# Optimization experiments

Hardware: AMD Instinct MI355X
Metric: run time of the kernel (lower is better)

Reference implementation:

```python
import jax, jax.numpy as jnp
import numpy as np

B, M, L, HID, H, LAYERS = 16, 128, 512, 256, 4, 2
DH = HID // H  # 64 = head dim, also kernel_param dim


def _ln(x, g, b, eps=1e-5):
    mu = jnp.mean(x, axis=-1, keepdims=True)
    var = jnp.mean((x - mu) ** 2, axis=-1, keepdims=True)
    return (x - mu) / jnp.sqrt(var + eps) * g + b


def setup_inputs() -> dict:
    key = jax.random.key(0)
    ks = jax.random.split(key, 24)
    s = 0.05
    return {
        "ct_t": jax.random.uniform(ks[0], (B, M), jnp.float32),
        "ts_t": jax.random.uniform(ks[1], (B, L), jnp.float32),
        "ct_emb": jax.random.normal(ks[2], (B, M, HID), jnp.float32),
        "ts_emb": jax.random.normal(ks[3], (B, L, HID), jnp.float32),
        "kernel_param": jax.random.normal(ks[4], (DH,), jnp.float32),
        "ct_W": jax.random.normal(ks[5], (HID, HID), jnp.float32) * s,
        "ct_b": jnp.zeros((HID,), jnp.float32),
        "fW0": jax.random.normal(ks[6], (HID, HID), jnp.float32) * s,
        "fb0": jnp.zeros((HID,), jnp.float32),
        "fW1": jax.random.normal(ks[7], (HID, HID), jnp.float32) * s,
        "fb1": jnp.zeros((HID,), jnp.float32),
        "fW2": jax.random.normal(ks[8], (HID, HID), jnp.float32) * s,
        "fb2": jnp.zeros((HID,), jnp.float32),
        "f_ln_g": jnp.ones((HID,), jnp.float32),
        "f_ln_b": jnp.zeros((HID,), jnp.float32),
        "Wqkv": jax.random.normal(ks[9], (LAYERS, 3 * HID, HID), jnp.float32) * s,
        "bqkv": jnp.zeros((LAYERS, 3 * HID), jnp.float32),
        "Wo": jax.random.normal(ks[10], (LAYERS, HID, HID), jnp.float32) * s,
        "bo": jnp.zeros((LAYERS, HID), jnp.float32),
        "W1": jax.random.normal(ks[11], (LAYERS, 2 * HID, HID), jnp.float32) * s,
        "b1": jnp.zeros((LAYERS, 2 * HID), jnp.float32),
        "W2": jax.random.normal(ks[12], (LAYERS, HID, 2 * HID), jnp.float32) * s,
        "b2": jnp.zeros((LAYERS, HID), jnp.float32),
        "ln1_g": jnp.ones((LAYERS, HID), jnp.float32),
        "ln1_b": jnp.zeros((LAYERS, HID), jnp.float32),
        "ln2_g": jnp.ones((LAYERS, HID), jnp.float32),
        "ln2_b": jnp.zeros((LAYERS, HID), jnp.float32),
        "pred_W": jax.random.normal(ks[13], (1, HID), jnp.float32) * s,
        "pred_b": jnp.zeros((1,), jnp.float32),
    }


def reference(ct_t, ts_t, ct_emb, ts_emb, kernel_param, ct_W, ct_b,
              fW0, fb0, fW1, fb1, fW2, fb2, f_ln_g, f_ln_b,
              Wqkv, bqkv, Wo, bo, W1, b1, W2, b2,
              ln1_g, ln1_b, ln2_g, ln2_b, pred_W, pred_b):
    # --- TN tokenizer: multi-scale RBF kernel temporal fusion ---
    alpha = jax.nn.softplus(kernel_param)                       # [DH]  log(1+exp(p))
    ct_e = (jnp.einsum('bmd,ed->bme', ct_emb, ct_W) + ct_b)     # [B,M,HID]
    ct_e = ct_e.reshape(B, M, H, DH)
    diff = ct_t[:, :, None] - ts_t[:, None, :]                  # [B,M,L]
    norm = (diff * diff)[..., None]                             # [B,M,L,1]
    outs = []
    for s in range(H):                                          # fixed small loop over scales
        z = (-float(s)) * alpha * norm                          # [B,M,L,DH]
        w = jax.nn.logsumexp(z, axis=3, keepdims=True)          # [B,M,L,1]
        sim = jnp.exp(z - w)                                    # normalized kernel sims
        outs.append(jnp.einsum('bmnd,bmd->bnd', sim, ct_e[:, :, s, :]))  # scatter over ts events
    temp = jnp.concatenate(outs, axis=-1)                       # [B,L,HID]
    # --- Fusion module ---
    aux = jax.nn.elu(temp @ fW0.T + fb0 + ts_emb @ fW1.T + fb1)
    x = _ln(aux @ fW2.T + fb2 + ts_emb, f_ln_g, f_ln_b)         # [B,L,HID]
    # --- Transformer encoder (post-LN, gelu, no dropout at eval) ---
    inv_sqrt = 1.0 / np.sqrt(DH).astype(np.float32)
    for l in range(LAYERS):
        qkv = x @ Wqkv[l].T + bqkv[l]                           # [B,L,3*HID]
        q, k, v = jnp.split(qkv, 3, axis=-1)
        def heads(t):
            return t.reshape(B, L, H, DH).transpose(0, 2, 1, 3)
        q, k, v = heads(q), heads(k), heads(v)
        att = jax.nn.softmax(jnp.einsum('bhqd,bhkd->bhqk', q, k) * inv_sqrt, axis=-1)
        o = jnp.einsum('bhqk,bhkd->bhqd', att, v).transpose(0, 2, 1, 3).reshape(B, L, HID)
        x = _ln(x + o @ Wo[l].T + bo[l], ln1_g[l], ln1_b[l])
        ff = jax.nn.gelu(x @ W1[l].T + b1[l], approximate=False) @ W2[l].T + b2[l]
        x = _ln(x + ff, ln2_g[l], ln2_b[l])
    return x @ pred_W.T + pred_b                                # [B,L,1]
```

## Files before the change

### kernel.cpp

```cpp
#include <hip/hip_runtime.h>
#include <hip/hip_bf16.h>
#include <cstddef>

#define Bsz 16
#define Msz 128
#define Lsz 512
#define HIDs 256

typedef __attribute__((ext_vector_type(4))) float f32x4;
typedef __attribute__((ext_vector_type(8))) __bf16 bf16x8;
typedef __attribute__((ext_vector_type(8))) unsigned short ushort8;

#define CHEB_K 12
#define PI_F 3.14159265358979323846f

static __device__ inline unsigned short f2bf(float f) {
    __hip_bfloat16 h = __float2bfloat16(f);
    return *(unsigned short*)&h;
}
static __device__ inline float bf2f(unsigned short u) {
    return __builtin_bit_cast(float, (unsigned)u << 16);
}
static __device__ inline void gload16(const ushort* g, ushort* l) {
    __builtin_amdgcn_global_load_lds(
        (const __attribute__((address_space(1))) void*)g,
        (__attribute__((address_space(3))) void*)l, 16, 0, 0);
}

__global__ __launch_bounds__(256) void cheb_kernel(
    const float* __restrict__ kp, float* __restrict__ clut, float* __restrict__ cD)
{
    __shared__ float costab[CHEB_K][32];
    __shared__ float xq[32];
    __shared__ float alph[64];
    const int t = threadIdx.x;
    if (t < 64) {
        float p = kp[t];
        alph[t] = fmaxf(p, 0.f) + log1pf(__expf(-fabsf(p)));
    }
    #pragma unroll
    for (int i = 0; i < 2; i++) {
        int idx = i * 256 + t;
        if (idx < CHEB_K * 32) {
            int k = idx >> 5, q = idx & 31;
            float th = (q + 0.5f) * (PI_F / 32.f);
            costab[k][q] = __cosf((float)k * th);
        }
    }
    if (t < 32) xq[t] = 0.5f * (1.f + __cosf((t + 0.5f) * (PI_F / 32.f)));
    __syncthreads();

    if (t >= 192) return;
    const int d = t & 63, s1 = t >> 6;
    const float u = (float)(s1 + 1) * alph[d];
    float f[32];
    #pragma unroll
    for (int q = 0; q < 32; q++) f[q] = __expf(-u * xq[q]);
    #pragma unroll
    for (int k = 0; k < CHEB_K; k++) {
        float sum = 0.f;
        #pragma unroll
        for (int q = 0; q < 32; q++) sum = fmaf(f[q], costab[k][q], sum);
        float c = sum * ((k == 0 ? 1.f : 2.f) / 32.f);
        clut[s1 * (CHEB_K * 64) + k * 64 + d] = c;
        float sr = c;
        #pragma unroll
        for (int o = 1; o <= 32; o <<= 1) sr += __shfl_xor(sr, o, 64);
        if (d == 0) cD[s1 * CHEB_K + k] = sr;
    }
}

__global__ __launch_bounds__(256) void prep_kernel(
    const float* __restrict__ ts_emb, const float* __restrict__ ct_emb,
    const float* __restrict__ ct_W, const float* __restrict__ fW0,
    const float* __restrict__ fW1, const float* __restrict__ fW2,
    const float* __restrict__ Wqkv, const float* __restrict__ Wo,
    const float* __restrict__ W1, const float* __restrict__ W2,
    ushort* __restrict__ Xcat, ushort* __restrict__ Wcat,
    ushort* __restrict__ cebin, ushort* __restrict__ wct,
    ushort* __restrict__ wf2, ushort* __restrict__ wqkv,
    ushort* __restrict__ wo, ushort* __restrict__ w1, ushort* __restrict__ w2,
    const float* __restrict__ ct_t, const float* __restrict__ ts_t,
    const float* __restrict__ cD, ushort* __restrict__ invW,
    const float* __restrict__ bqkv, float* __restrict__ bqs)
{
    const int bid = blockIdx.x;
    const int tid = threadIdx.x;

    if (bid < 1920) {
        const unsigned u = bid * 256u + tid;
        const float* src; ushort* dst; unsigned rel;
        float sc = 1.f;
        if (u < 262144u) {
            rel = u; src = ts_emb;
            dst = Xcat + ((size_t)(rel >> 5) * 512 + 256 + (rel & 31) * 8);
        } else if (u < 327680u) { rel = u - 262144u; src = ct_emb; dst = cebin + (size_t)rel * 8; }
        else if (u < 335872u) { rel = u - 327680u; src = ct_W; dst = wct + (size_t)rel * 8; }
        else if (u < 344064u) { rel = u - 335872u; src = fW0;
            dst = Wcat + ((size_t)(rel >> 5) * 512 + (rel & 31) * 8); }
        else if (u < 352256u) { rel = u - 344064u; src = fW1;
            dst = Wcat + ((size_t)(rel >> 5) * 512 + 256 + (rel & 31) * 8); }
        else if (u < 360448u) { rel = u - 352256u; src = fW2; dst = wf2 + (size_t)rel * 8; }
        else if (u < 409600u) { rel = u - 360448u; src = Wqkv; dst = wqkv + (size_t)rel * 8;
            if (((rel >> 5) % 768) < 256) sc = 0.125f; }
        else if (u < 425984u) { rel = u - 409600u; src = Wo;  dst = wo + (size_t)rel * 8; }
        else if (u < 458752u) { rel = u - 425984u; src = W1;  dst = w1 + (size_t)rel * 8; }
        else                  { rel = u - 458752u; src = W2;  dst = w2 + (size_t)rel * 8; }
        float4 a = ((const float4*)src)[(size_t)rel * 2];
        float4 b = ((const float4*)src)[(size_t)rel * 2 + 1];
        ushort8 o;
        o[0] = f2bf(a.x * sc); o[1] = f2bf(a.y * sc); o[2] = f2bf(a.z * sc); o[3] = f2bf(a.w * sc);
        o[4] = f2bf(b.x * sc); o[5] = f2bf(b.y * sc); o[6] = f2bf(b.z * sc); o[7] = f2bf(b.w * sc);
        *(ushort8*)dst = o;
    } else if (bid < 6016) {
        __shared__ float cd[3][CHEB_K];
        if (tid < 3 * CHEB_K) cd[tid / CHEB_K][tid % CHEB_K] = cD[tid];
        __syncthreads();

        const unsigned G = (bid - 1920) * 256u + tid;
        const int b = G >> 16;
        const int n = (G >> 7) & 511;
        const int m = G & 127;

        float x = ct_t[b * Msz + m] - ts_t[b * Lsz + n];
        x = x * x;
        const float xi = 2.f * x - 1.f;
        const float xi2 = 2.f * xi;

        float t0 = 1.f, t1 = xi;
        float a1 = cd[0][0] + cd[0][1] * xi;
        float a2 = cd[1][0] + cd[1][1] * xi;
        float a3 = cd[2][0] + cd[2][1] * xi;
        #pragma unroll
        for (int k = 2; k < CHEB_K; k++) {
            float tn = fmaf(xi2, t1, -t0);
            a1 = fmaf(cd[0][k], tn, a1);
            a2 = fmaf(cd[1][k], tn, a2);
            a3 = fmaf(cd[2][k], tn, a3);
            t0 = t1; t1 = tn;
        }
        const size_t base = ((size_t)b * 3 * Lsz + n) * Msz + m;
        invW[base]                         = f2bf(1.f / a1);
        invW[base + (size_t)Lsz * Msz]     = f2bf(1.f / a2);
        invW[base + (size_t)2 * Lsz * Msz] = f2bf(1.f / a3);
    } else {
        #pragma unroll
        for (int i = 0; i < 6; i++) {
            int idx = i * 256 + tid;
            int c = idx % 768;
            bqs[idx] = bqkv[idx] * ((c < 256) ? 0.125f : 1.f);
        }
    }
}

__global__ __launch_bounds__(256) void gemm_mfma_kernel(
    const ushort* __restrict__ X, const ushort* __restrict__ W,
    const float* __restrict__ bias, const float* __restrict__ bias2,
    ushort* __restrict__ Yb, int NR, int K, int OUT, int act)
{
    __shared__ ushort As[2][64 * 64];
    __shared__ ushort Bs[2][128 * 64];

    const int nbx = OUT >> 7;
    const int bx = blockIdx.x % nbx;
    const int by = blockIdx.x / nbx;
    const int r0 = by << 6, o0 = bx << 7;
    const int tid = threadIdx.x;
    const int w = tid >> 6;
    const int lane = tid & 63;
    const int wr = w >> 1, wc = w & 1;
    const int lr = lane & 15, lg = lane >> 4;

    const int grow = lane >> 3;
    const int gchunk = (lane & 7) ^ grow;

    unsigned aoff[2][2], boff[4][2];
    #pragma unroll
    for (int f = 0; f < 2; f++) {
        unsigned cc = (unsigned)((lg + 4 * f) ^ (lr & 7)) * 16u;
        #pragma unroll
        for (int m = 0; m < 2; m++)
            aoff[m][f] = (unsigned)(wr * 32 + m * 16 + lr) * 128u + cc;
        #pragma unroll
        for (int n = 0; n < 4; n++)
            boff[n][f] = (unsigned)(wc * 64 + n * 16 + lr) * 128u + cc;
    }

    f32x4 acc[2][4];
    #pragma unroll
    for (int m = 0; m < 2; m++)
        #pragma unroll
        for (int n = 0; n < 4; n++) acc[m][n] = (f32x4){0.f, 0.f, 0.f, 0.f};

    const int nk = K >> 6;

    auto stage = [&](int buf, int ks) {
        const int k0 = ks << 6;
        #pragma unroll
        for (int i = 0; i < 2; i++) {
            int row = w * 16 + i * 8 + grow;
            gload16(X + (size_t)(r0 + row) * K + k0 + gchunk * 8,
                    &As[buf][(w * 16 + i * 8) * 64]);
        }
        #pragma unroll
        for (int i = 0; i < 4; i++) {
            int row = w * 32 + i * 8 + grow;
            gload16(W + (size_t)(o0 + row) * K + k0 + gchunk * 8,
                    &Bs[buf][(w * 32 + i * 8) * 64]);
        }
    };

    stage(0, 0);
    __syncthreads();
    int cur = 0;
    for (int ks = 0; ks < nk; ks++) {
        if (ks + 1 < nk) stage(cur ^ 1, ks + 1);
        const char* Ab = (const char*)As[cur];
        const char* Bb = (const char*)Bs[cur];
        #pragma unroll
        for (int f = 0; f < 2; f++) {
            bf16x8 av[2], bv[4];
            #pragma unroll
            for (int m = 0; m < 2; m++)
                av[m] = *(const bf16x8*)(Ab + aoff[m][f]);
            #pragma unroll
            for (int n = 0; n < 4; n++)
                bv[n] = *(const bf16x8*)(Bb + boff[n][f]);
            #pragma unroll
            for (int m = 0; m < 2; m++)
                #pragma unroll
                for (int n = 0; n < 4; n++)
                    acc[m][n] = __builtin_amdgcn_mfma_f32_16x16x32_bf16(
                        av[m], bv[n], acc[m][n], 0, 0, 0);
        }
        __syncthreads();
        cur ^= 1;
    }

    const int ocol0 = o0 + wc * 64;
    float bn[4];
    #pragma unroll
    for (int n = 0; n < 4; n++) {
        int o = ocol0 + n * 16 + lr;
        bn[n] = bias[o] + (bias2 ? bias2[o] : 0.f);
    }

    #pragma unroll
    for (int m = 0; m < 2; m++) {
        #pragma unroll
        for (int p = 0; p < 4; p++) {
            int r = r0 + wr * 32 + m * 16 + 4 * lg + p;
            size_t rb = (size_t)r * OUT;
            #pragma unroll
            for (int n = 0; n < 4; n++) {
                int o = ocol0 + n * 16 + lr;
                float v = acc[m][n][p] + bn[n];
                if (act == 1)      v = (v > 0.f) ? v : (__expf(v) - 1.f);
                else if (act == 2) v = 0.5f * v * (1.f + erff(v * 0.70710678118654752f));
                Yb[rb + o] = f2bf(v);
            }
        }
    }
}

__global__ __launch_bounds__(256) void gemm_ln_kernel(
    const ushort* __restrict__ X, const ushort* __restrict__ W,
    const float* __restrict__ bias, const ushort* __restrict__ add,
    int addS, int addO,
    const float* __restrict__ lng, const float* __restrict__ lnb,
    ushort* __restrict__ Xb,
    const float* __restrict__ predW, const float* __restrict__ predb,
    float* __restrict__ pout, int K)
{
    __shared__ ushort As[2][16 * 64];
    __shared__ ushort Bs[2][256 * 64];
    __shared__ float redA[16][4];
    __shared__ float redB[16][4];

    const int r0 = blockIdx.x << 4;
    const int tid = threadIdx.x;
    const int w = tid >> 6;
    const int lane = tid & 63;
    const int lr = lane & 15, lg = lane >> 4;
    const int grow = lane >> 3;
    const int gchunk = (lane & 7) ^ grow;

    unsigned aoff[2], boff[4][2];
    #pragma unroll
    for (int f = 0; f < 2; f++) {
        unsigned cc = (unsigned)((lg + 4 * f) ^ (lr & 7)) * 16u;
        aoff[f] = (unsigned)lr * 128u + cc;
        #pragma unroll
        for (int n = 0; n < 4; n++)
            boff[n][f] = (unsigned)(w * 64 + n * 16 + lr) * 128u + cc;
    }

    f32x4 acc[4];
    #pragma unroll
    for (int n = 0; n < 4; n++) acc[n] = (f32x4){0.f, 0.f, 0.f, 0.f};

    const int nk = K >> 6;

    auto stage = [&](int buf, int ks) {
        const int k0 = ks << 6;
        if (w < 2)
            gload16(X + (size_t)(r0 + w * 8 + grow) * K + k0 + gchunk * 8,
                    &As[buf][(w * 8) * 64]);
        #pragma unroll
        for (int i = 0; i < 8; i++) {
            gload16(W + (size_t)(w * 64 + i * 8 + grow) * K + k0 + gchunk * 8,
                    &Bs[buf][(w * 64 + i * 8) * 64]);
        }
    };

    stage(0, 0);
    __syncthreads();
    int cur = 0;
    for (int ks = 0; ks < nk; ks++) {
        if (ks + 1 < nk) stage(cur ^ 1, ks + 1);
        const char* Ab = (const char*)As[cur];
        const char* Bb = (const char*)Bs[cur];
        #pragma unroll
        for (int f = 0; f < 2; f++) {
            bf16x8 av = *(const bf16x8*)(Ab + aoff[f]);
            #pragma unroll
            for (int n = 0; n < 4; n++) {
                bf16x8 bv = *(const bf16x8*)(Bb + boff[n][f]);
                acc[n] = __builtin_amdgcn_mfma_f32_16x16x32_bf16(
                    av, bv, acc[n], 0, 0, 0);
            }
        }
        __syncthreads();
        cur ^= 1;
    }

    const int col0 = w * 64;
    float bn[4], gv[4], bv2[4], pwv[4];
    #pragma unroll
    for (int n = 0; n < 4; n++) {
        int o = col0 + n * 16 + lr;
        bn[n] = bias[o];
        gv[n] = lng[o];
        bv2[n] = lnb[o];
        pwv[n] = predW ? predW[o] : 0.f;
    }
    #pragma unroll
    for (int p = 0; p < 4; p++) {
        size_t ra = (size_t)(r0 + 4 * lg + p) * addS + addO;
        #pragma unroll
        for (int n = 0; n < 4; n++)
            acc[n][p] += bn[n] + bf2f(add[ra + col0 + n * 16 + lr]);
    }

    #pragma unroll
    for (int p = 0; p < 4; p++) {
        float s = acc[0][p] + acc[1][p] + acc[2][p] + acc[3][p];
        #pragma unroll
        for (int o = 1; o <= 8; o <<= 1) s += __shfl_xor(s, o);
        if (lr == 0) redA[4 * lg + p][w] = s;
    }
    __syncthreads();
    float mu[4];
    #pragma unroll
    for (int p = 0; p < 4; p++) {
        int row = 4 * lg + p;
        mu[p] = (redA[row][0] + redA[row][1] + redA[row][2] + redA[row][3]) * (1.f / 256.f);
    }

    #pragma unroll
    for (int p = 0; p < 4; p++) {
        float q = 0.f;
        #pragma unroll
        for (int n = 0; n < 4; n++) {
            float dl = acc[n][p] - mu[p];
            q = fmaf(dl, dl, q);
        }
        #pragma unroll
        for (int o = 1; o <= 8; o <<= 1) q += __shfl_xor(q, o);
        if (lr == 0) redB[4 * lg + p][w] = q;
    }
    __syncthreads();

    #pragma unroll
    for (int p = 0; p < 4; p++) {
        int row = 4 * lg + p;
        float var = (redB[row][0] + redB[row][1] + redB[row][2] + redB[row][3]) * (1.f / 256.f);
        float rsig = rsqrtf(var + 1e-5f);
        size_t rb = (size_t)(r0 + row) * 256;
        float pd = 0.f;
        #pragma unroll
        for (int n = 0; n < 4; n++) {
            int o = col0 + n * 16 + lr;
            float xn = (acc[n][p] - mu[p]) * rsig * gv[n] + bv2[n];
            if (Xb) Xb[rb + o] = f2bf(xn);
            pd = fmaf(xn, pwv[n], pd);
        }
        if (predW) {
            #pragma unroll
            for (int o = 1; o <= 8; o <<= 1) pd += __shfl_xor(pd, o);
            if (lr == 0) redA[row][w] = pd;
        }
    }
    if (predW) {
        __syncthreads();
        if (tid < 16)
            pout[r0 + tid] = redA[tid][0] + redA[tid][1] + redA[tid][2]
                           + redA[tid][3] + predb[0];
    }
}

__global__ __launch_bounds__(256) void tokmix_kernel(
    const float* __restrict__ ct_t, const float* __restrict__ ts_t,
    const ushort* __restrict__ ceb, const ushort* __restrict__ invW,
    const float* __restrict__ clut, ushort* __restrict__ Xcat)
{
    const int bid = blockIdx.x;
    const int tid = threadIdx.x;

    if (bid < 384) {
        const int nt = bid & 7;
        const int s1 = (bid >> 3) % 3;
        const int b  = bid / 24;
        const int w = tid >> 6, lane = tid & 63, g = lane >> 4, r = lane & 15;

        __shared__ ushort ceT[64][136];
        __shared__ float  cl[CHEB_K][64];
        __shared__ float  cts[128];

        #pragma unroll
        for (int i = 0; i < 8; i++) {
            int idx = i * 256 + tid;
            int m = idx >> 4, d4 = (idx & 15) << 2;
            const ushort* gp = ceb + (((size_t)b * 128 + m) << 8) + (s1 + 1) * 64 + d4;
            ushort4 v = *(const ushort4*)gp;
            ceT[d4 + 0][m] = v.x; ceT[d4 + 1][m] = v.y;
            ceT[d4 + 2][m] = v.z; ceT[d4 + 3][m] = v.w;
        }
        #pragma unroll
        for (int i = 0; i < 3; i++) {
            int idx = i * 256 + tid;
            cl[idx >> 6][idx & 63] = clut[s1 * (CHEB_K * 64) + idx];
        }
        if (tid < 128) cts[tid] = ct_t[b * 128 + tid];
        __syncthreads();

        const int nrow = nt * 64 + w * 16 + r;
        const float tsn = ts_t[b * 512 + nrow];

        float xi2v[4][8], Ta[4][8], Tb[4][8];
        #pragma unroll
        for (int t4 = 0; t4 < 4; t4++) {
            int m0 = 8 * g + 32 * t4;
            ushort8 iv = *(const ushort8*)&invW[((((size_t)b * 3 + s1) * 512 + nrow) << 7) + m0];
            #pragma unroll
            for (int j = 0; j < 8; j++) {
                float dfx = cts[m0 + j] - tsn;
                float x = dfx * dfx;
                float xi = 2.f * x - 1.f;
                float w0 = bf2f(iv[j]);
                xi2v[t4][j] = 2.f * xi;
                Ta[t4][j] = w0;
                Tb[t4][j] = w0 * xi;
            }
        }

        bf16x8 cef[4][4];
        #pragma unroll
        for (int db = 0; db < 4; db++)
            #pragma unroll
            for (int t4 = 0; t4 < 4; t4++)
                cef[db][t4] = *(const bf16x8*)&ceT[db * 16 + r][8 * g + 32 * t4];

        f32x4 acc[4];
        #pragma unroll
        for (int db = 0; db < 4; db++) acc[db] = (f32x4){0.f, 0.f, 0.f, 0.f};

        #pragma unroll
        for (int k = 0; k < CHEB_K; k++) {
            if (k >= 2) {
                #pragma unroll
                for (int t4 = 0; t4 < 4; t4++)
                    #pragma unroll
                    for (int j = 0; j < 8; j++) {
                        if (k & 1) Tb[t4][j] = fmaf(xi2v[t4][j], Ta[t4][j], -Tb[t4][j]);
                        else       Ta[t4][j] = fmaf(xi2v[t4][j], Tb[t4][j], -Ta[t4][j]);
                    }
            }
            bf16x8 af[4];
            #pragma unroll
            for (int t4 = 0; t4 < 4; t4++) {
                ushort8 u;
                #pragma unroll
                for (int j = 0; j < 8; j++)
                    u[j] = f2bf((k & 1) ? Tb[t4][j] : Ta[t4][j]);
                af[t4] = __builtin_bit_cast(bf16x8, u);
            }
            #pragma unroll
            for (int db = 0; db < 4; db++) {
                f32x4 gk = (f32x4){0.f, 0.f, 0.f, 0.f};
                #pragma unroll
                for (int t4 = 0; t4 < 4; t4++)
                    gk = __builtin_amdgcn_mfma_f32_16x16x32_bf16(af[t4], cef[db][t4], gk, 0, 0, 0);
                float ck = cl[k][db * 16 + r];
                #pragma unroll
                for (int p = 0; p < 4; p++) acc[db][p] = fmaf(ck, gk[p], acc[db][p]);
            }
        }

        #pragma unroll
        for (int db = 0; db < 4; db++)
            #pragma unroll
            for (int p = 0; p < 4; p++) {
                int n_out = nt * 64 + w * 16 + 4 * g + p;
                Xcat[((size_t)b * 512 + n_out) * 512 + (s1 + 1) * 64 + db * 16 + r] =
                    f2bf(acc[db][p]);
            }
    } else {
        const int b = bid - 384;
        const int d = tid & 63, q = tid >> 6;
        float s = 0.f;
        #pragma unroll 8
        for (int i = 0; i < 32; i++) {
            int m = q * 32 + i;
            s += bf2f(ceb[(((size_t)b * 128 + m) << 8) + d]);
        }
        __shared__ float red0[4][64];
        __shared__ ushort row0[64];
        red0[q][d] = s;
        __syncthreads();
        if (tid < 64)
            row0[tid] = f2bf((red0[0][tid] + red0[1][tid] + red0[2][tid] + red0[3][tid])
                             * (1.f / 64.f));
        __syncthreads();
        #pragma unroll
        for (int i = 0; i < 16; i++) {
            int idx = i * 256 + tid;
            int n = idx >> 3, j = idx & 7;
            *(ushort8*)&Xcat[((size_t)b * 512 + n) * 512 + j * 8] =
                *(const ushort8*)&row0[j * 8];
        }
    }
}

__global__ __launch_bounds__(256) void attn_mfma_kernel(
    const ushort* __restrict__ qkv, ushort* __restrict__ Ob)
{
    const int bid = blockIdx.x;
    const int qt = bid & 7;
    const int h  = (bid >> 3) & 3;
    const int b  = bid >> 5;
    const int t  = threadIdx.x;
    const int w  = t >> 6;
    const int lane = t & 63;
    const int g = lane >> 4;
    const int r = lane & 15;

    __shared__ ushort Ks[64][72];
    __shared__ ushort Vt[64][72];
    __shared__ float  Ps[4][16][65];

    const ushort* base = qkv + (size_t)b * Lsz * 768;
    const int q0 = qt * 64 + w * 16;

    bf16x8 qf[2];
    {
        const ushort* qp = base + (size_t)(q0 + r) * 768 + h * 64 + 8 * g;
        qf[0] = __builtin_bit_cast(bf16x8, *(const ushort8*)qp);
        qf[1] = __builtin_bit_cast(bf16x8, *(const ushort8*)(qp + 32));
    }

    f32x4 Ofr[4];
    #pragma unroll
    for (int dblk = 0; dblk < 4; dblk++) Ofr[dblk] = (f32x4){0.f, 0.f, 0.f, 0.f};
    float m_run[4] = {-1e30f, -1e30f, -1e30f, -1e30f};
    float l_run[4] = {0.f, 0.f, 0.f, 0.f};

    const int srow = t >> 2;
    const int sseg = t & 3;

    ushort8 pk0, pk1, pv0, pv1;
    auto gload_chunk = [&](int c) {
        const ushort* kr = base + (size_t)(c * 64 + srow) * 768 + 256 + h * 64 + sseg * 16;
        pk0 = *(const ushort8*)kr;
        pk1 = *(const ushort8*)(kr + 8);
        pv0 = *(const ushort8*)(kr + 256);
        pv1 = *(const ushort8*)(kr + 264);
    };
    auto write_chunk = [&]() {
        *(ushort8*)&Ks[srow][sseg * 16]     = pk0;
        *(ushort8*)&Ks[srow][sseg * 16 + 8] = pk1;
        #pragma unroll
        for (int j = 0; j < 8; j++) {
            Vt[sseg * 16 + j][srow]     = pv0[j];
            Vt[sseg * 16 + 8 + j][srow] = pv1[j];
        }
    };

    gload_chunk(0);
    write_chunk();
    __syncthreads();

    for (int c = 0; c < 8; c++) {
        if (c < 7) gload_chunk(c + 1);

        f32x4 sfr[4];
        #pragma unroll
        for (int s = 0; s < 4; s++) {
            f32x4 a2 = (f32x4){0.f, 0.f, 0.f, 0.f};
            #pragma unroll
            for (int f = 0; f < 2; f++) {
                bf16x8 kf = *(const bf16x8*)&Ks[s * 16 + r][8 * g + 32 * f];
                a2 = __builtin_amdgcn_mfma_f32_16x16x32_bf16(qf[f], kf, a2, 0, 0, 0);
            }
            sfr[s] = a2;
        }

        #pragma unroll
        for (int p = 0; p < 4; p++) {
            float rm = fmaxf(fmaxf(sfr[0][p], sfr[1][p]), fmaxf(sfr[2][p], sfr[3][p]));
            #pragma unroll
            for (int o = 1; o <= 8; o <<= 1) rm = fmaxf(rm, __shfl_xor(rm, o));
            float mnew = fmaxf(m_run[p], rm);
            float sc = __expf(m_run[p] - mnew);
            m_run[p] = mnew;
            float rs = 0.f;
            #pragma unroll
            for (int s = 0; s < 4; s++) {
                float pv = __expf(sfr[s][p] - mnew);
                Ps[w][4 * g + p][s * 16 + r] = pv;
                rs += pv;
            }
            #pragma unroll
            for (int o = 1; o <= 8; o <<= 1) rs += __shfl_xor(rs, o);
            l_run[p] = l_run[p] * sc + rs;
            #pragma unroll
            for (int dblk = 0; dblk < 4; dblk++) Ofr[dblk][p] *= sc;
        }

        __asm__ volatile("s_waitcnt lgkmcnt(0)" ::: "memory");

        #pragma unroll
        for (int f = 0; f < 2; f++) {
            const float* pp = &Ps[w][r][8 * g + 32 * f];
            ushort8 ua;
            #pragma unroll
            for (int j = 0; j < 8; j++) ua[j] = f2bf(pp[j]);
            bf16x8 pa = __builtin_bit_cast(bf16x8, ua);
            #pragma unroll
            for (int dblk = 0; dblk < 4; dblk++) {
                bf16x8 vb = *(const bf16x8*)&Vt[dblk * 16 + r][32 * f + 8 * g];
                Ofr[dblk] = __builtin_amdgcn_mfma_f32_16x16x32_bf16(
                    pa, vb, Ofr[dblk], 0, 0, 0);
            }
        }

        __syncthreads();
        if (c < 7) {
            write_chunk();
            __syncthreads();
        }
    }

    #pragma unroll
    for (int dblk = 0; dblk < 4; dblk++) {
        #pragma unroll
        for (int p = 0; p < 4; p++) {
            int row = q0 + 4 * g + p;
            Ob[(size_t)(b * Lsz + row) * HIDs + h * 64 + dblk * 16 + r] =
                f2bf(Ofr[dblk][p] / l_run[p]);
        }
    }
}

extern "C" void kernel_launch(void* const* d_in, const int* in_sizes, int n_in,
                              void* d_out, int out_size, void* d_ws, size_t ws_size,
                              hipStream_t stream)
{
    (void)in_sizes; (void)n_in; (void)out_size; (void)ws_size;

    const float* ct_t   = (const float*)d_in[0];
    const float* ts_t   = (const float*)d_in[1];
    const float* ct_emb = (const float*)d_in[2];
    const float* ts_emb = (const float*)d_in[3];
    const float* kp     = (const float*)d_in[4];
    const float* ct_W   = (const float*)d_in[5];
    const float* ct_b   = (const float*)d_in[6];
    const float* fW0    = (const float*)d_in[7];
    const float* fb0    = (const float*)d_in[8];
    const float* fW1    = (const float*)d_in[9];
    const float* fb1    = (const float*)d_in[10];
    const float* fW2    = (const float*)d_in[11];
    const float* fb2    = (const float*)d_in[12];
    const float* f_ln_g = (const float*)d_in[13];
    const float* f_ln_b = (const float*)d_in[14];
    const float* Wqkv   = (const float*)d_in[15];
    const float* bqkv   = (const float*)d_in[16];
    const float* Wo     = (const float*)d_in[17];
    const float* bo     = (const float*)d_in[18];
    const float* W1     = (const float*)d_in[19];
    const float* b1     = (const float*)d_in[20];
    const float* W2     = (const float*)d_in[21];
    const float* b2     = (const float*)d_in[22];
    const float* ln1_g  = (const float*)d_in[23];
    const float* ln1_b  = (const float*)d_in[24];
    const float* ln2_g  = (const float*)d_in[25];
    const float* ln2_b  = (const float*)d_in[26];
    const float* pred_W = (const float*)d_in[27];
    const float* pred_b = (const float*)d_in[28];

    ushort* wsb = (ushort*)d_ws;
    ushort* invW  = wsb;
    ushort* auxbf = wsb;
    ushort* qkvbf = wsb;
    ushort* ff1bf = wsb;
    ushort* Xcat  = wsb + 12582912;
    ushort* Wcat  = wsb + 16777216;
    ushort* cebin = wsb + 16908288;
    ushort* cebout= wsb + 17432576;
    ushort* wct   = wsb + 17956864;
    ushort* wf2   = wsb + 18022400;
    ushort* wqkv  = wsb + 18087936;
    ushort* wo    = wsb + 18481152;
    ushort* w1    = wsb + 18612224;
    ushort* w2    = wsb + 18874368;
    ushort* xbf   = wsb + 19136512;
    ushort* obf   = wsb + 21233664;
    float*  wsf   = (float*)d_ws;
    float*  clut  = wsf + 11665408;
    float*  cDp   = wsf + 11667712;
    float*  bqs   = wsf + 11667776;

    const int NRts = Bsz * Lsz;
    const int NRct = Bsz * Msz;
    auto grid = [](int nr, int out) { return dim3((unsigned)((nr >> 6) * (out >> 7))); };

    cheb_kernel<<<dim3(1), 256, 0, stream>>>(kp, clut, cDp);
    prep_kernel<<<dim3(1920 + 4096 + 1), 256, 0, stream>>>(
        ts_emb, ct_emb, ct_W, fW0, fW1, fW2, Wqkv, Wo, W1, W2,
        Xcat, Wcat, cebin, wct, wf2, wqkv, wo, w1, w2,
        ct_t, ts_t, cDp, invW, bqkv, bqs);

    gemm_mfma_kernel<<<grid(NRct, 256), 256, 0, stream>>>(
        cebin, wct, ct_b, nullptr, cebout, NRct, 256, 256, 0);
    tokmix_kernel<<<dim3(400), 256, 0, stream>>>(ct_t, ts_t, cebout, invW, clut, Xcat);

    gemm_mfma_kernel<<<grid(NRts, 256), 256, 0, stream>>>(
        Xcat, Wcat, fb0, fb1, auxbf, NRts, 512, 256, 1);
    gemm_ln_kernel<<<dim3(NRts / 16), 256, 0, stream>>>(
        auxbf, wf2, fb2, Xcat, 512, 256, f_ln_g, f_ln_b, xbf,
        nullptr, nullptr, nullptr, 256);

    for (int l = 0; l < 2; l++) {
        gemm_mfma_kernel<<<grid(NRts, 768), 256, 0, stream>>>(
            xbf, wqkv + (size_t)l * 196608, bqs + l * 768, nullptr,
            qkvbf, NRts, 256, 768, 0);
        attn_mfma_kernel<<<dim3(512), 256, 0, stream>>>(qkvbf, obf);
        gemm_ln_kernel<<<dim3(NRts / 16), 256, 0, stream>>>(
            obf, wo + (size_t)l * 65536, bo + l * 256, xbf, 256, 0,
            ln1_g + l * 256, ln1_b + l * 256, xbf,
            nullptr, nullptr, nullptr, 256);
        gemm_mfma_kernel<<<grid(NRts, 512), 256, 0, stream>>>(
            xbf, w1 + (size_t)l * 131072, b1 + l * 512, nullptr,
            ff1bf, NRts, 256, 512, 2);
        if (l == 0) {
            gemm_ln_kernel<<<dim3(NRts / 16), 256, 0, stream>>>(
                ff1bf, w2 + (size_t)l * 131072, b2 + l * 256, xbf, 256, 0,
                ln2_g + l * 256, ln2_b + l * 256, xbf,
                nullptr, nullptr, nullptr, 512);
        } else {
            gemm_ln_kernel<<<dim3(NRts / 16), 256, 0, stream>>>(
                ff1bf, w2 + (size_t)l * 131072, b2 + l * 256, xbf, 256, 0,
                ln2_g + l * 256, ln2_b + l * 256, nullptr,
                pred_W, pred_b, (float*)d_out, 512);
        }
    }
}
```

Measured before the change: 197.5 us.

## Enlarge gemm_ln row tile to 32 and attention key chunks to 128

The fused GEMM+LayerNorm kernel now handles 32 rows per block with 512 threads. Two groups of four waves share each staged weight tile, which halves the redundant weight loads per row. The attention kernel now processes 128-key chunks in 4 iterations instead of 64-key chunks in 8, cutting loop and barrier overhead. It also raises wave priority around the MFMA sections. In exchange, LDS use grows in both kernels, which may lower occupancy, and the gemm_ln grid has half as many blocks.

```diff
diff --git a/kernel.cpp b/kernel.cpp
--- a/kernel.cpp
+++ b/kernel.cpp
@@ -263,7 +263,7 @@
     }
 }
 
-__global__ __launch_bounds__(256) void gemm_ln_kernel(
+__global__ __launch_bounds__(512) void gemm_ln_kernel(
     const ushort* __restrict__ X, const ushort* __restrict__ W,
     const float* __restrict__ bias, const ushort* __restrict__ add,
     int addS, int addO,
@@ -272,16 +272,18 @@
     const float* __restrict__ predW, const float* __restrict__ predb,
     float* __restrict__ pout, int K)
 {
-    __shared__ ushort As[2][16 * 64];
+    __shared__ ushort As[2][32 * 64];
     __shared__ ushort Bs[2][256 * 64];
-    __shared__ float redA[16][4];
-    __shared__ float redB[16][4];
-
-    const int r0 = blockIdx.x << 4;
+    __shared__ float redA[32][4];
+    __shared__ float redB[32][4];
+
+    const int r0 = blockIdx.x << 5;
     const int tid = threadIdx.x;
     const int w = tid >> 6;
     const int lane = tid & 63;
     const int lr = lane & 15, lg = lane >> 4;
+    const int wg = w >> 2;
+    const int ws = w & 3;
     const int grow = lane >> 3;
     const int gchunk = (lane & 7) ^ grow;
 
@@ -289,10 +291,10 @@
     #pragma unroll
     for (int f = 0; f < 2; f++) {
         unsigned cc = (unsigned)((lg + 4 * f) ^ (lr & 7)) * 16u;
-        aoff[f] = (unsigned)lr * 128u + cc;
+        aoff[f] = (unsigned)(wg * 16 + lr) * 128u + cc;
         #pragma unroll
         for (int n = 0; n < 4; n++)
-            boff[n][f] = (unsigned)(w * 64 + n * 16 + lr) * 128u + cc;
+            boff[n][f] = (unsigned)(ws * 64 + n * 16 + lr) * 128u + cc;
     }
 
     f32x4 acc[4];
@@ -303,13 +305,13 @@
 
     auto stage = [&](int buf, int ks) {
         const int k0 = ks << 6;
-        if (w < 2)
+        if (w < 4)
             gload16(X + (size_t)(r0 + w * 8 + grow) * K + k0 + gchunk * 8,
                     &As[buf][(w * 8) * 64]);
         #pragma unroll
-        for (int i = 0; i < 8; i++) {
-            gload16(W + (size_t)(w * 64 + i * 8 + grow) * K + k0 + gchunk * 8,
-                    &Bs[buf][(w * 64 + i * 8) * 64]);
+        for (int i = 0; i < 4; i++) {
+            gload16(W + (size_t)(w * 32 + i * 8 + grow) * K + k0 + gchunk * 8,
+                    &Bs[buf][(w * 32 + i * 8) * 64]);
         }
     };
 
@@ -334,7 +336,7 @@
         cur ^= 1;
     }
 
-    const int col0 = w * 64;
+    const int col0 = ws * 64;
     float bn[4], gv[4], bv2[4], pwv[4];
     #pragma unroll
     for (int n = 0; n < 4; n++) {
@@ -346,7 +348,7 @@
     }
     #pragma unroll
     for (int p = 0; p < 4; p++) {
-        size_t ra = (size_t)(r0 + 4 * lg + p) * addS + addO;
+        size_t ra = (size_t)(r0 + wg * 16 + 4 * lg + p) * addS + addO;
         #pragma unroll
         for (int n = 0; n < 4; n++)
             acc[n][p] += bn[n] + bf2f(add[ra + col0 + n * 16 + lr]);
@@ -357,13 +359,13 @@
         float s = acc[0][p] + acc[1][p] + acc[2][p] + acc[3][p];
         #pragma unroll
         for (int o = 1; o <= 8; o <<= 1) s += __shfl_xor(s, o);
-        if (lr == 0) redA[4 * lg + p][w] = s;
+        if (lr == 0) redA[wg * 16 + 4 * lg + p][ws] = s;
     }
     __syncthreads();
     float mu[4];
     #pragma unroll
     for (int p = 0; p < 4; p++) {
-        int row = 4 * lg + p;
+        int row = wg * 16 + 4 * lg + p;
         mu[p] = (redA[row][0] + redA[row][1] + redA[row][2] + redA[row][3]) * (1.f / 256.f);
     }
 
@@ -377,13 +379,13 @@
         }
         #pragma unroll
         for (int o = 1; o <= 8; o <<= 1) q += __shfl_xor(q, o);
-        if (lr == 0) redB[4 * lg + p][w] = q;
+        if (lr == 0) redB[wg * 16 + 4 * lg + p][ws] = q;
     }
     __syncthreads();
 
     #pragma unroll
     for (int p = 0; p < 4; p++) {
-        int row = 4 * lg + p;
+        int row = wg * 16 + 4 * lg + p;
         float var = (redB[row][0] + redB[row][1] + redB[row][2] + redB[row][3]) * (1.f / 256.f);
         float rsig = rsqrtf(var + 1e-5f);
         size_t rb = (size_t)(r0 + row) * 256;
@@ -398,12 +400,12 @@
         if (predW) {
             #pragma unroll
             for (int o = 1; o <= 8; o <<= 1) pd += __shfl_xor(pd, o);
-            if (lr == 0) redA[row][w] = pd;
+            if (lr == 0) redA[row][ws] = pd;
         }
     }
     if (predW) {
         __syncthreads();
-        if (tid < 16)
+        if (tid < 32)
             pout[r0 + tid] = redA[tid][0] + redA[tid][1] + redA[tid][2]
                            + redA[tid][3] + predb[0];
     }
@@ -555,9 +557,9 @@
     const int g = lane >> 4;
     const int r = lane & 15;
 
-    __shared__ ushort Ks[64][72];
-    __shared__ ushort Vt[64][72];
-    __shared__ float  Ps[4][16][65];
+    __shared__ ushort Ks[128][72];
+    __shared__ ushort Vt[64][136];
+    __shared__ float  Ps[4][16][129];
 
     const ushort* base = qkv + (size_t)b * Lsz * 768;
     const int q0 = qt * 64 + w * 16;
@@ -575,24 +577,25 @@
     float m_run[4] = {-1e30f, -1e30f, -1e30f, -1e30f};
     float l_run[4] = {0.f, 0.f, 0.f, 0.f};
 
-    const int srow = t >> 2;
-    const int sseg = t & 3;
-
-    ushort8 pk0, pk1, pv0, pv1;
+    const int srow = t >> 1;
+    const int sseg = t & 1;
+
+    ushort8 pk[4], pv[4];
     auto gload_chunk = [&](int c) {
-        const ushort* kr = base + (size_t)(c * 64 + srow) * 768 + 256 + h * 64 + sseg * 16;
-        pk0 = *(const ushort8*)kr;
-        pk1 = *(const ushort8*)(kr + 8);
-        pv0 = *(const ushort8*)(kr + 256);
-        pv1 = *(const ushort8*)(kr + 264);
+        const ushort* kr = base + (size_t)(c * 128 + srow) * 768 + 256 + h * 64 + sseg * 32;
+        #pragma unroll
+        for (int i = 0; i < 4; i++) {
+            pk[i] = *(const ushort8*)(kr + 8 * i);
+            pv[i] = *(const ushort8*)(kr + 256 + 8 * i);
+        }
     };
     auto write_chunk = [&]() {
-        *(ushort8*)&Ks[srow][sseg * 16]     = pk0;
-        *(ushort8*)&Ks[srow][sseg * 16 + 8] = pk1;
-        #pragma unroll
-        for (int j = 0; j < 8; j++) {
-            Vt[sseg * 16 + j][srow]     = pv0[j];
-            Vt[sseg * 16 + 8 + j][srow] = pv1[j];
+        #pragma unroll
+        for (int i = 0; i < 4; i++) {
+            *(ushort8*)&Ks[srow][sseg * 32 + 8 * i] = pk[i];
+            #pragma unroll
+            for (int j = 0; j < 8; j++)
+                Vt[sseg * 32 + 8 * i + j][srow] = pv[i][j];
         }
     };
 
@@ -600,12 +603,13 @@
     write_chunk();
     __syncthreads();
 
-    for (int c = 0; c < 8; c++) {
-        if (c < 7) gload_chunk(c + 1);
-
-        f32x4 sfr[4];
-        #pragma unroll
-        for (int s = 0; s < 4; s++) {
+    for (int c = 0; c < 4; c++) {
+        if (c < 3) gload_chunk(c + 1);
+
+        f32x4 sfr[8];
+        __builtin_amdgcn_s_setprio(1);
+        #pragma unroll
+        for (int s = 0; s < 8; s++) {
             f32x4 a2 = (f32x4){0.f, 0.f, 0.f, 0.f};
             #pragma unroll
             for (int f = 0; f < 2; f++) {
@@ -614,10 +618,13 @@
             }
             sfr[s] = a2;
         }
+        __builtin_amdgcn_s_setprio(0);
 
         #pragma unroll
         for (int p = 0; p < 4; p++) {
-            float rm = fmaxf(fmaxf(sfr[0][p], sfr[1][p]), fmaxf(sfr[2][p], sfr[3][p]));
+            float rm = sfr[0][p];
+            #pragma unroll
+            for (int s = 1; s < 8; s++) rm = fmaxf(rm, sfr[s][p]);
             #pragma unroll
             for (int o = 1; o <= 8; o <<= 1) rm = fmaxf(rm, __shfl_xor(rm, o));
             float mnew = fmaxf(m_run[p], rm);
@@ -625,10 +632,10 @@
             m_run[p] = mnew;
             float rs = 0.f;
             #pragma unroll
-            for (int s = 0; s < 4; s++) {
-                float pv = __expf(sfr[s][p] - mnew);
-                Ps[w][4 * g + p][s * 16 + r] = pv;
-                rs += pv;
+            for (int s = 0; s < 8; s++) {
+                float pvx = __expf(sfr[s][p] - mnew);
+                Ps[w][4 * g + p][s * 16 + r] = pvx;
+                rs += pvx;
             }
             #pragma unroll
             for (int o = 1; o <= 8; o <<= 1) rs += __shfl_xor(rs, o);
@@ -640,22 +647,24 @@
         __asm__ volatile("s_waitcnt lgkmcnt(0)" ::: "memory");
 
         #pragma unroll
-        for (int f = 0; f < 2; f++) {
-            const float* pp = &Ps[w][r][8 * g + 32 * f];
+        for (int ks2 = 0; ks2 < 4; ks2++) {
+            const float* pp = &Ps[w][r][8 * g + 32 * ks2];
             ushort8 ua;
             #pragma unroll
             for (int j = 0; j < 8; j++) ua[j] = f2bf(pp[j]);
             bf16x8 pa = __builtin_bit_cast(bf16x8, ua);
+            __builtin_amdgcn_s_setprio(1);
             #pragma unroll
             for (int dblk = 0; dblk < 4; dblk++) {
-                bf16x8 vb = *(const bf16x8*)&Vt[dblk * 16 + r][32 * f + 8 * g];
+                bf16x8 vb = *(const bf16x8*)&Vt[dblk * 16 + r][32 * ks2 + 8 * g];
                 Ofr[dblk] = __builtin_amdgcn_mfma_f32_16x16x32_bf16(
                     pa, vb, Ofr[dblk], 0, 0, 0);
             }
+            __builtin_amdgcn_s_setprio(0);
         }
 
         __syncthreads();
-        if (c < 7) {
+        if (c < 3) {
             write_chunk();
             __syncthreads();
         }
@@ -746,7 +755,7 @@
 
     gemm_mfma_kernel<<<grid(NRts, 256), 256, 0, stream>>>(
         Xcat, Wcat, fb0, fb1, auxbf, NRts, 512, 256, 1);
-    gemm_ln_kernel<<<dim3(NRts / 16), 256, 0, stream>>>(
+    gemm_ln_kernel<<<dim3(NRts / 32), 512, 0, stream>>>(
         auxbf, wf2, fb2, Xcat, 512, 256, f_ln_g, f_ln_b, xbf,
         nullptr, nullptr, nullptr, 256);
 
@@ -755,7 +764,7 @@
             xbf, wqkv + (size_t)l * 196608, bqs + l * 768, nullptr,
             qkvbf, NRts, 256, 768, 0);
         attn_mfma_kernel<<<dim3(512), 256, 0, stream>>>(qkvbf, obf);
-        gemm_ln_kernel<<<dim3(NRts / 16), 256, 0, stream>>>(
+        gemm_ln_kernel<<<dim3(NRts / 32), 512, 0, stream>>>(
             obf, wo + (size_t)l * 65536, bo + l * 256, xbf, 256, 0,
             ln1_g + l * 256, ln1_b + l * 256, xbf,
             nullptr, nullptr, nullptr, 256);
@@ -763,12 +772,12 @@
             xbf, w1 + (size_t)l * 131072, b1 + l * 512, nullptr,
             ff1bf, NRts, 256, 512, 2);
         if (l == 0) {
-            gemm_ln_kernel<<<dim3(NRts / 16), 256, 0, stream>>>(
+            gemm_ln_kernel<<<dim3(NRts / 32), 512, 0, stream>>>(
                 ff1bf, w2 + (size_t)l * 131072, b2 + l * 256, xbf, 256, 0,
                 ln2_g + l * 256, ln2_b + l * 256, xbf,
                 nullptr, nullptr, nullptr, 512);
         } else {
-            gemm_ln_kernel<<<dim3(NRts / 16), 256, 0, stream>>>(
+            gemm_ln_kernel<<<dim3(NRts / 32), 512, 0, stream>>>(
                 ff1bf, w2 + (size_t)l * 131072, b2 + l * 256, xbf, 256, 0,
                 ln2_g + l * 256, ln2_b + l * 256, nullptr,
                 pred_W, pred_b, (float*)d_out, 512);
```

After: 190.0 us. 1.04x faster.
